# Performance work log

Hardware: AMD Instinct MI355X
Metric: run time of the kernel (lower is better)

## Reference

```python
import jax, jax.numpy as jnp
import numpy as np

IN_FEATURES = 1024
OUT_FEATURES = 256
GRID_SIZE = 5
SPLINE_ORDER = 3
SCALE_BASE = 1.0
GRID_RANGE = (-1.0, 1.0)


def make_grid():
    h = (GRID_RANGE[1] - GRID_RANGE[0]) / GRID_SIZE
    g = jnp.arange(-SPLINE_ORDER, GRID_SIZE + SPLINE_ORDER + 1, dtype=jnp.float32) * h + GRID_RANGE[0]
    # (in_features, grid_size + 2*spline_order + 1) = (1024, 12)
    return jnp.broadcast_to(g[None, :], (IN_FEATURES, g.shape[0]))


def setup_inputs() -> dict:
    key = jax.random.key(0)
    k1, k2, k3 = jax.random.split(key, 3)
    batch = 16384
    x = jax.random.normal(k1, (batch, IN_FEATURES), dtype=jnp.float32)
    base_weight = jax.random.normal(k2, (OUT_FEATURES, IN_FEATURES), dtype=jnp.float32) * 0.03
    n_basis = GRID_SIZE + SPLINE_ORDER  # 8
    spline_weight = (jax.random.uniform(k3, (OUT_FEATURES, IN_FEATURES * n_basis), dtype=jnp.float32) - 0.5) * 0.1 / n_basis
    grid = make_grid()
    return {"x": x, "base_weight": base_weight, "spline_weight": spline_weight, "grid": grid}


def b_splines(x, grid):
    # x: (B, F) -> (B, F, grid_size + spline_order)
    xe = x[:, :, None]  # (B, F, 1)
    bases = ((xe >= grid[:, :-1]) & (xe < grid[:, 1:])).astype(x.dtype)
    for k in range(1, SPLINE_ORDER + 1):
        left = (xe - grid[:, : -(k + 1)]) / (grid[:, k:-1] - grid[:, : -(k + 1)])
        right = (grid[:, k + 1 :] - xe) / (grid[:, k + 1 :] - grid[:, 1:-k])
        bases = left * bases[:, :, :-1] + right * bases[:, :, 1:]
    return bases.reshape(x.shape[0], -1)  # (B, F*(grid_size+spline_order))


def reference(x, base_weight, spline_weight, grid):
    base_out = jax.nn.silu(x) @ (base_weight * SCALE_BASE).T  # (B, out)
    spline_basis = b_splines(x, grid)                          # (B, F*8)
    spline_out = spline_basis @ spline_weight.T                # (B, out)
    return base_out + spline_out
```

## Files before the change

### kernel.cpp

```cpp
#include <hip/hip_runtime.h>
#include <cstdint>
#include <cstddef>

typedef unsigned short u16;
typedef unsigned int   u32;
typedef unsigned long long u64;
typedef __attribute__((ext_vector_type(8))) short short8;
typedef __attribute__((ext_vector_type(4))) float f32x4;

#define M_ROWS 16384
#define N_COLS 256
#define IN_F   1024
#define K_SPL  8192
#define K_TOT  9216
#define NCHUNK 144
#define SPLITK 2
#define CPB    (NCHUNK / SPLITK)

__device__ __forceinline__ u32 f2bf1(float f) {
  u32 u = __float_as_uint(f);
  u += 0x7fffu + ((u >> 16) & 1u);
  return u >> 16;
}
__device__ __forceinline__ u32 pk2(float a, float b) {
  return f2bf1(a) | (f2bf1(b) << 16);
}
__device__ __forceinline__ float silu(float v) {
  return v * __builtin_amdgcn_rcpf(1.f + __expf(-v));
}

__device__ __forceinline__ uint4 basis8(float xv) {
  float u = fmaf(xv, 2.5f, 5.5f);
  int i0 = (int)u;
  float fr = u - (float)i0;
  float fr2 = fr * fr, fr3 = fr2 * fr;
  float om  = 1.f - fr;
  float om3 = om * om * om;
  float w0 = om3 * (1.f / 6.f);
  float w3 = fr3 * (1.f / 6.f);
  float w1 = fmaf(fr3, 0.5f, fmaf(fr2, -1.f, 2.f / 3.f));
  float w2 = fmaf(fr + fr2 - fr3, 0.5f, 1.f / 6.f);
  u64 W = (u64)pk2(w0, w1) | ((u64)pk2(w2, w3) << 32);
  if (!(u >= 0.f && u < 11.f)) W = 0ull;
  int s = (i0 - 3) * 16;
  u64 lo, hi;
  if (s >= 64)      { int r = s - 64; lo = 0ull; hi = (r < 64) ? (W << r) : 0ull; }
  else if (s > 0)   { lo = W << s;    hi = W >> (64 - s); }
  else if (s == 0)  { lo = W;         hi = 0ull; }
  else              { int r = -s;     lo = (r < 64) ? (W >> r) : 0ull; hi = 0ull; }
  uint4 o;
  o.x = (u32)lo; o.y = (u32)(lo >> 32); o.z = (u32)hi; o.w = (u32)(hi >> 32);
  return o;
}

__global__ void pack_weights(const float* __restrict__ bw, const float* __restrict__ sw,
                             u16* __restrict__ Bp) {
  int o  = blockIdx.y;
  int k4 = (blockIdx.x * blockDim.x + threadIdx.x) * 4;
  const float* src = (k4 < K_SPL) ? (sw + (size_t)o * K_SPL + k4)
                                  : (bw + (size_t)o * IN_F + (k4 - K_SPL));
  float a = src[0], b = src[1], c = src[2], d = src[3];
  uint2 v; v.x = pk2(a, b); v.y = pk2(c, d);
  *(uint2*)(Bp + (size_t)o * K_TOT + k4) = v;
}

__global__ __launch_bounds__(512, 4)
void kan_gemm(const float* __restrict__ x, const u16* __restrict__ Bp,
              float* __restrict__ out) {
  __shared__ __align__(16) u16 As[64 * 64];
  __shared__ __align__(16) u16 Bs[256 * 64];

  const int tid  = threadIdx.x;
  const int lane = tid & 63;
  const int w    = tid >> 6;
  const int wm   = w & 1;
  const int wn   = w >> 1;

  const int bid  = blockIdx.x;
  const int kid  = bid & 1;
  const int mb   = bid >> 1;
  const int row0 = mb * 64;
  const int cs   = kid * CPB, c1 = cs + CPB;

  f32x4 acc[2][4];
#pragma unroll
  for (int i = 0; i < 2; ++i)
#pragma unroll
    for (int j = 0; j < 4; ++j)
      acc[i][j] = (f32x4){0.f, 0.f, 0.f, 0.f};

  const int sr = tid >> 3;
  const int sq = tid & 7;

  const int lm = lane & 15;
  const int kg = lane >> 4;
  int a_off[2][2], b_off[2][4];
#pragma unroll
  for (int h = 0; h < 2; ++h) {
    int c = h * 4 + kg;
#pragma unroll
    for (int i = 0; i < 2; ++i) {
      int ra = wm * 32 + i * 16 + lm;
      a_off[h][i] = ra * 64 + ((c ^ (ra & 7)) * 8);
    }
#pragma unroll
    for (int j = 0; j < 4; ++j) {
      int rb = wn * 64 + j * 16 + lm;
      b_off[h][j] = rb * 64 + ((c ^ (rb & 7)) * 8);
    }
  }

  float px;
  float4 pb0, pb1;

  auto LOADX = [&](int c) {
    if (c < 128) {
      px = x[(size_t)(row0 + sr) * IN_F + c * 8 + sq];
    } else {
      const float* xp = x + (size_t)(row0 + sr) * IN_F + (c - 128) * 64 + sq * 8;
      pb0 = *(const float4*)xp;
      pb1 = *(const float4*)(xp + 4);
    }
  };

  auto BUILD = [&](int c) {
    uint4 q;
    if (c < 128) {
      q = basis8(px);
    } else {
      q.x = pk2(silu(pb0.x), silu(pb0.y));
      q.y = pk2(silu(pb0.z), silu(pb0.w));
      q.z = pk2(silu(pb1.x), silu(pb1.y));
      q.w = pk2(silu(pb1.z), silu(pb1.w));
    }
    *(uint4*)(As + sr * 64 + ((sq ^ (sr & 7)) * 8)) = q;
  };

  auto STAGEB = [&](int c) {
#pragma unroll
    for (int it = 0; it < 4; ++it) {
      int s = tid + it * 512;
      int r_ = s >> 3, cc = (s & 7) ^ (r_ & 7);
      const u16* gp = Bp + (size_t)r_ * K_TOT + c * 64 + cc * 8;
      __builtin_amdgcn_global_load_lds((const __attribute__((address_space(1))) void*)gp,
                                       (__attribute__((address_space(3))) void*)(Bs + s * 8),
                                       16, 0, 0);
    }
  };

  LOADX(cs);
  for (int c = cs; c < c1; ++c) {
    BUILD(c);
    STAGEB(c);
    if (c + 1 < c1) LOADX(c + 1);
    __syncthreads();
#pragma unroll
    for (int h = 0; h < 2; ++h) {
      short8 af[2], bf[4];
#pragma unroll
      for (int i = 0; i < 2; ++i) af[i] = *(const short8*)(As + a_off[h][i]);
#pragma unroll
      for (int j = 0; j < 4; ++j) bf[j] = *(const short8*)(Bs + b_off[h][j]);
#pragma unroll
      for (int i = 0; i < 2; ++i)
#pragma unroll
        for (int j = 0; j < 4; ++j)
          acc[i][j] = __builtin_amdgcn_mfma_f32_16x16x32_bf16(af[i], bf[j], acc[i][j], 0, 0, 0);
    }
    __syncthreads();
  }

  const int lc = lane & 15;
  const int lr = (lane >> 4) * 4;
#pragma unroll
  for (int i = 0; i < 2; ++i) {
#pragma unroll
    for (int j = 0; j < 4; ++j) {
      int gr = row0 + wm * 32 + i * 16 + lr;
      int gc = wn * 64 + j * 16 + lc;
      float* po = out + (size_t)gr * N_COLS + gc;
#pragma unroll
      for (int r = 0; r < 4; ++r)
        unsafeAtomicAdd(po + (size_t)r * N_COLS, acc[i][j][r]);
    }
  }
}

extern "C" void kernel_launch(void* const* d_in, const int* in_sizes, int n_in,
                              void* d_out, int out_size, void* d_ws, size_t ws_size,
                              hipStream_t stream) {
  const float* x  = (const float*)d_in[0];
  const float* bw = (const float*)d_in[1];
  const float* sw = (const float*)d_in[2];
  float* out = (float*)d_out;
  u16* Bp = (u16*)d_ws;

  hipMemsetAsync(d_out, 0, (size_t)M_ROWS * N_COLS * sizeof(float), stream);

  dim3 pgrid(K_TOT / 4 / 256, N_COLS);
  pack_weights<<<pgrid, 256, 0, stream>>>(bw, sw, Bp);

  kan_gemm<<<512, 512, 0, stream>>>(x, Bp, out);
}
```

Baseline: 212.0 us.

## Double-buffer A and B LDS tiles to overlap staging with MFMA

Adds a second LDS buffer for the A and B tiles and restructures the K loop as a two-stage ping-pong. The next chunk's B tile (async global_load_lds) and basis/SiLU A tile are prepared while MFMAs run on the current buffer, and one of the two barriers per chunk is removed. LDS use doubles to about 80 KB per block, which may reduce how many blocks fit on a CU compared with the launch_bounds target.

```diff
diff --git a/kernel.cpp b/kernel.cpp
--- a/kernel.cpp
+++ b/kernel.cpp
@@ -67,8 +67,8 @@
 __global__ __launch_bounds__(512, 4)
 void kan_gemm(const float* __restrict__ x, const u16* __restrict__ Bp,
               float* __restrict__ out) {
-  __shared__ __align__(16) u16 As[64 * 64];
-  __shared__ __align__(16) u16 Bs[256 * 64];
+  __shared__ __align__(16) u16 Bs[2 * 256 * 64];
+  __shared__ __align__(16) u16 As[2 * 64 * 64];
 
   const int tid  = threadIdx.x;
   const int lane = tid & 63;
@@ -123,7 +123,7 @@
     }
   };
 
-  auto BUILD = [&](int c) {
+  auto BUILD = [&](int c, int buf) {
     uint4 q;
     if (c < 128) {
       q = basis8(px);
@@ -133,41 +133,58 @@
       q.z = pk2(silu(pb1.x), silu(pb1.y));
       q.w = pk2(silu(pb1.z), silu(pb1.w));
     }
-    *(uint4*)(As + sr * 64 + ((sq ^ (sr & 7)) * 8)) = q;
-  };
-
-  auto STAGEB = [&](int c) {
+    *(uint4*)(As + buf * (64 * 64) + sr * 64 + ((sq ^ (sr & 7)) * 8)) = q;
+  };
+
+  auto STAGEB = [&](int c, int buf) {
+    u16* base = Bs + buf * (256 * 64);
 #pragma unroll
     for (int it = 0; it < 4; ++it) {
       int s = tid + it * 512;
       int r_ = s >> 3, cc = (s & 7) ^ (r_ & 7);
       const u16* gp = Bp + (size_t)r_ * K_TOT + c * 64 + cc * 8;
       __builtin_amdgcn_global_load_lds((const __attribute__((address_space(1))) void*)gp,
-                                       (__attribute__((address_space(3))) void*)(Bs + s * 8),
+                                       (__attribute__((address_space(3))) void*)(base + s * 8),
                                        16, 0, 0);
     }
   };
 
-  LOADX(cs);
-  for (int c = cs; c < c1; ++c) {
-    BUILD(c);
-    STAGEB(c);
-    if (c + 1 < c1) LOADX(c + 1);
-    __syncthreads();
+  auto MFMA_PHASE = [&](int buf) {
+    const u16* Ab = As + buf * (64 * 64);
+    const u16* Bb = Bs + buf * (256 * 64);
 #pragma unroll
     for (int h = 0; h < 2; ++h) {
       short8 af[2], bf[4];
 #pragma unroll
-      for (int i = 0; i < 2; ++i) af[i] = *(const short8*)(As + a_off[h][i]);
-#pragma unroll
-      for (int j = 0; j < 4; ++j) bf[j] = *(const short8*)(Bs + b_off[h][j]);
+      for (int i = 0; i < 2; ++i) af[i] = *(const short8*)(Ab + a_off[h][i]);
+#pragma unroll
+      for (int j = 0; j < 4; ++j) bf[j] = *(const short8*)(Bb + b_off[h][j]);
 #pragma unroll
       for (int i = 0; i < 2; ++i)
 #pragma unroll
         for (int j = 0; j < 4; ++j)
           acc[i][j] = __builtin_amdgcn_mfma_f32_16x16x32_bf16(af[i], bf[j], acc[i][j], 0, 0, 0);
     }
+  };
+
+  LOADX(cs);
+  STAGEB(cs, 0);
+  BUILD(cs, 0);
+  if (cs + 1 < c1) LOADX(cs + 1);
+  __syncthreads();
+
+  for (int c = cs; c < c1; c += 2) {
+    if (c + 1 < c1) { STAGEB(c + 1, 1); BUILD(c + 1, 1); }
+    if (c + 2 < c1) LOADX(c + 2);
+    MFMA_PHASE(0);
     __syncthreads();
+
+    if (c + 1 < c1) {
+      if (c + 2 < c1) { STAGEB(c + 2, 0); BUILD(c + 2, 0); }
+      if (c + 3 < c1) LOADX(c + 3);
+      MFMA_PHASE(1);
+      __syncthreads();
+    }
   }
 
   const int lc = lane & 15;
```

Result: faster. 204.7 us (-3.5%).

## Pipeline kan_gemm with 4-stage LDS ring, 1024 threads, K=32 chunks

Applied to the files above, without the earlier changes.

Blocks grow to 1024 threads (16 waves, each computing a 32x32 tile), and the K chunk drops to 32. A 4-slot LDS ring buffer lets B staging run three chunks ahead and A basis building run two chunks ahead, split across thread quarters. This replaces the two __syncthreads per chunk with one barrier plus explicit vmcnt waits. The aim is to overlap global loads and basis computation with MFMA and to cut barrier stalls. In exchange each wave reuses less data per fragment, there are twice as many barriers overall, and the hand-written waitcnt logic adds fragility.

```diff
diff --git a/kernel.cpp b/kernel.cpp
--- a/kernel.cpp
+++ b/kernel.cpp
@@ -13,7 +13,7 @@
 #define IN_F   1024
 #define K_SPL  8192
 #define K_TOT  9216
-#define NCHUNK 144
+#define NCHUNK 288
 #define SPLITK 2
 #define CPB    (NCHUNK / SPLITK)
 
@@ -64,11 +64,11 @@
   *(uint2*)(Bp + (size_t)o * K_TOT + k4) = v;
 }
 
-__global__ __launch_bounds__(512, 4)
+__global__ __launch_bounds__(1024, 8)
 void kan_gemm(const float* __restrict__ x, const u16* __restrict__ Bp,
               float* __restrict__ out) {
-  __shared__ __align__(16) u16 As[64 * 64];
-  __shared__ __align__(16) u16 Bs[256 * 64];
+  __shared__ __align__(16) u16 Bs[4 * 256 * 32];
+  __shared__ __align__(16) u16 As[4 * 64 * 32];
 
   const int tid  = threadIdx.x;
   const int lane = tid & 63;
@@ -82,92 +82,105 @@
   const int row0 = mb * 64;
   const int cs   = kid * CPB, c1 = cs + CPB;
 
-  f32x4 acc[2][4];
+  f32x4 acc[2][2];
 #pragma unroll
   for (int i = 0; i < 2; ++i)
 #pragma unroll
-    for (int j = 0; j < 4; ++j)
+    for (int j = 0; j < 2; ++j)
       acc[i][j] = (f32x4){0.f, 0.f, 0.f, 0.f};
 
-  const int sr = tid >> 3;
-  const int sq = tid & 7;
+  const int q    = tid >> 8;
+  const int loc  = tid & 255;
+  const int brow = loc >> 2;
+  const int bq   = loc & 3;
+  const int a_wr = brow * 32 + ((bq ^ ((brow >> 1) & 3)) * 8);
 
   const int lm = lane & 15;
   const int kg = lane >> 4;
-  int a_off[2][2], b_off[2][4];
-#pragma unroll
-  for (int h = 0; h < 2; ++h) {
-    int c = h * 4 + kg;
-#pragma unroll
-    for (int i = 0; i < 2; ++i) {
-      int ra = wm * 32 + i * 16 + lm;
-      a_off[h][i] = ra * 64 + ((c ^ (ra & 7)) * 8);
-    }
-#pragma unroll
-    for (int j = 0; j < 4; ++j) {
-      int rb = wn * 64 + j * 16 + lm;
-      b_off[h][j] = rb * 64 + ((c ^ (rb & 7)) * 8);
-    }
-  }
+  int a_off[2], b_off[2];
+#pragma unroll
+  for (int i = 0; i < 2; ++i) {
+    int ra = wm * 32 + i * 16 + lm;
+    a_off[i] = ra * 32 + ((kg ^ ((ra >> 1) & 3)) * 8);
+  }
+#pragma unroll
+  for (int j = 0; j < 2; ++j) {
+    int rb = wn * 32 + j * 16 + lm;
+    b_off[j] = rb * 32 + ((kg ^ ((rb >> 1) & 3)) * 8);
+  }
+
+  const u32 stage_goff = (u32)(tid >> 2) * K_TOT + (((tid & 3) ^ ((tid >> 3) & 3)) * 8);
+  const int stage_loff = tid * 8;
 
   float px;
   float4 pb0, pb1;
 
   auto LOADX = [&](int c) {
-    if (c < 128) {
-      px = x[(size_t)(row0 + sr) * IN_F + c * 8 + sq];
+    if ((c & 3) != q) return;
+    if (c < 256) {
+      px = x[(size_t)(row0 + brow) * IN_F + c * 4 + bq];
     } else {
-      const float* xp = x + (size_t)(row0 + sr) * IN_F + (c - 128) * 64 + sq * 8;
+      const float* xp = x + (size_t)(row0 + brow) * IN_F + (c - 256) * 32 + bq * 8;
       pb0 = *(const float4*)xp;
       pb1 = *(const float4*)(xp + 4);
     }
   };
 
   auto BUILD = [&](int c) {
-    uint4 q;
-    if (c < 128) {
-      q = basis8(px);
+    if ((c & 3) != q) return;
+    uint4 v;
+    if (c < 256) {
+      v = basis8(px);
     } else {
-      q.x = pk2(silu(pb0.x), silu(pb0.y));
-      q.y = pk2(silu(pb0.z), silu(pb0.w));
-      q.z = pk2(silu(pb1.x), silu(pb1.y));
-      q.w = pk2(silu(pb1.z), silu(pb1.w));
+      v.x = pk2(silu(pb0.x), silu(pb0.y));
+      v.y = pk2(silu(pb0.z), silu(pb0.w));
+      v.z = pk2(silu(pb1.x), silu(pb1.y));
+      v.w = pk2(silu(pb1.z), silu(pb1.w));
     }
-    *(uint4*)(As + sr * 64 + ((sq ^ (sr & 7)) * 8)) = q;
+    *(uint4*)(As + (c & 3) * (64 * 32) + a_wr) = v;
   };
 
   auto STAGEB = [&](int c) {
-#pragma unroll
-    for (int it = 0; it < 4; ++it) {
-      int s = tid + it * 512;
-      int r_ = s >> 3, cc = (s & 7) ^ (r_ & 7);
-      const u16* gp = Bp + (size_t)r_ * K_TOT + c * 64 + cc * 8;
-      __builtin_amdgcn_global_load_lds((const __attribute__((address_space(1))) void*)gp,
-                                       (__attribute__((address_space(3))) void*)(Bs + s * 8),
-                                       16, 0, 0);
-    }
+    const u16* gp = Bp + stage_goff + c * 32;
+    __builtin_amdgcn_global_load_lds((const __attribute__((address_space(1))) void*)gp,
+                                     (__attribute__((address_space(3))) void*)
+                                       (Bs + (c & 3) * (256 * 32) + stage_loff),
+                                     16, 0, 0);
   };
 
-  LOADX(cs);
+  LOADX(cs); LOADX(cs + 1); LOADX(cs + 2);
+  asm volatile("s_waitcnt vmcnt(0)" ::: "memory");
+  BUILD(cs); BUILD(cs + 1); BUILD(cs + 2);
+  STAGEB(cs); STAGEB(cs + 1); STAGEB(cs + 2);
+  asm volatile("s_waitcnt vmcnt(2) lgkmcnt(0)" ::: "memory");
+  __builtin_amdgcn_s_barrier();
+
   for (int c = cs; c < c1; ++c) {
-    BUILD(c);
-    STAGEB(c);
-    if (c + 1 < c1) LOADX(c + 1);
-    __syncthreads();
-#pragma unroll
-    for (int h = 0; h < 2; ++h) {
-      short8 af[2], bf[4];
-#pragma unroll
-      for (int i = 0; i < 2; ++i) af[i] = *(const short8*)(As + a_off[h][i]);
-#pragma unroll
-      for (int j = 0; j < 4; ++j) bf[j] = *(const short8*)(Bs + b_off[h][j]);
-#pragma unroll
-      for (int i = 0; i < 2; ++i)
-#pragma unroll
-        for (int j = 0; j < 4; ++j)
-          acc[i][j] = __builtin_amdgcn_mfma_f32_16x16x32_bf16(af[i], bf[j], acc[i][j], 0, 0, 0);
-    }
-    __syncthreads();
+    const u16* Ab = As + (c & 3) * (64 * 32);
+    const u16* Bb = Bs + (c & 3) * (256 * 32);
+    short8 af[2], bf[2];
+#pragma unroll
+    for (int i = 0; i < 2; ++i) af[i] = *(const short8*)(Ab + a_off[i]);
+#pragma unroll
+    for (int j = 0; j < 2; ++j) bf[j] = *(const short8*)(Bb + b_off[j]);
+
+    if (c + 3 < c1) STAGEB(c + 3);
+    if (c + 2 < c1) BUILD(c + 2);
+    if (c + 3 < c1) LOADX(c + 3);
+
+    const int rem = c1 - c;
+    if (rem >= 4)      asm volatile("s_waitcnt vmcnt(3) lgkmcnt(0)" ::: "memory");
+    else if (rem == 3) asm volatile("s_waitcnt vmcnt(2) lgkmcnt(0)" ::: "memory");
+    else               asm volatile("s_waitcnt vmcnt(0) lgkmcnt(0)" ::: "memory");
+    __builtin_amdgcn_s_barrier();
+
+    __builtin_amdgcn_s_setprio(1);
+#pragma unroll
+    for (int i = 0; i < 2; ++i)
+#pragma unroll
+      for (int j = 0; j < 2; ++j)
+        acc[i][j] = __builtin_amdgcn_mfma_f32_16x16x32_bf16(af[i], bf[j], acc[i][j], 0, 0, 0);
+    __builtin_amdgcn_s_setprio(0);
   }
 
   const int lc = lane & 15;
@@ -175,9 +188,9 @@
 #pragma unroll
   for (int i = 0; i < 2; ++i) {
 #pragma unroll
-    for (int j = 0; j < 4; ++j) {
+    for (int j = 0; j < 2; ++j) {
       int gr = row0 + wm * 32 + i * 16 + lr;
-      int gc = wn * 64 + j * 16 + lc;
+      int gc = wn * 32 + j * 16 + lc;
       float* po = out + (size_t)gr * N_COLS + gc;
 #pragma unroll
       for (int r = 0; r < 4; ++r)
@@ -200,5 +213,5 @@
   dim3 pgrid(K_TOT / 4 / 256, N_COLS);
   pack_weights<<<pgrid, 256, 0, stream>>>(bw, sw, Bp);
 
-  kan_gemm<<<512, 512, 0, stream>>>(x, Bp, out);
-}
+  kan_gemm<<<512, 1024, 0, stream>>>(x, Bp, out);
+}
```

Result: slower. 234.2 us (+10.5%).

## Double-buffer LDS tiles and enlarge M tile to 128 rows

Applied to the files above, without the earlier changes.

The GEMM tile grows from 64 to 128 rows per block, so each block holds a 4x4 grid of MFMA accumulators per wave and the B tile is reused across twice as many rows. A and B shared-memory buffers are double-buffered: the next B tile is staged asynchronously and the next A tile is built while the current MFMAs run, using manual vmcnt waits and a single barrier per iteration. MFMA sections are raised in priority with s_setprio. The cost is more LDS and registers, which lowers occupancy, and half as many blocks (256), which may underfill the GPU's compute units.

```diff
diff --git a/kernel.cpp b/kernel.cpp
--- a/kernel.cpp
+++ b/kernel.cpp
@@ -64,11 +64,11 @@
   *(uint2*)(Bp + (size_t)o * K_TOT + k4) = v;
 }
 
-__global__ __launch_bounds__(512, 4)
+__global__ __launch_bounds__(512, 2)
 void kan_gemm(const float* __restrict__ x, const u16* __restrict__ Bp,
               float* __restrict__ out) {
-  __shared__ __align__(16) u16 As[64 * 64];
-  __shared__ __align__(16) u16 Bs[256 * 64];
+  __shared__ __align__(16) u16 Bs[2 * 256 * 64];
+  __shared__ __align__(16) u16 As[2 * 128 * 64];
 
   const int tid  = threadIdx.x;
   const int lane = tid & 63;
@@ -79,104 +79,143 @@
   const int bid  = blockIdx.x;
   const int kid  = bid & 1;
   const int mb   = bid >> 1;
-  const int row0 = mb * 64;
+  const int row0 = mb * 128;
   const int cs   = kid * CPB, c1 = cs + CPB;
 
-  f32x4 acc[2][4];
-#pragma unroll
-  for (int i = 0; i < 2; ++i)
+  f32x4 acc[4][4];
+#pragma unroll
+  for (int i = 0; i < 4; ++i)
 #pragma unroll
     for (int j = 0; j < 4; ++j)
       acc[i][j] = (f32x4){0.f, 0.f, 0.f, 0.f};
 
-  const int sr = tid >> 3;
-  const int sq = tid & 7;
+  const int br = tid >> 2;
+  const int bq = tid & 3;
+  const int a_wr0 = br * 64 + ((bq ^ (br & 7)) * 8);
+  const int a_wr1 = br * 64 + (((bq + 4) ^ (br & 7)) * 8);
 
   const int lm = lane & 15;
   const int kg = lane >> 4;
-  int a_off[2][2], b_off[2][4];
-#pragma unroll
-  for (int h = 0; h < 2; ++h) {
-    int c = h * 4 + kg;
-#pragma unroll
-    for (int i = 0; i < 2; ++i) {
-      int ra = wm * 32 + i * 16 + lm;
-      a_off[h][i] = ra * 64 + ((c ^ (ra & 7)) * 8);
-    }
-#pragma unroll
-    for (int j = 0; j < 4; ++j) {
-      int rb = wn * 64 + j * 16 + lm;
-      b_off[h][j] = rb * 64 + ((c ^ (rb & 7)) * 8);
-    }
-  }
-
-  float px;
-  float4 pb0, pb1;
+  int a_off[4], b_off[4];
+#pragma unroll
+  for (int i = 0; i < 4; ++i) {
+    int ra = wm * 64 + i * 16 + lm;
+    a_off[i] = ra * 64 + ((kg ^ (ra & 7)) * 8);
+  }
+#pragma unroll
+  for (int j = 0; j < 4; ++j) {
+    int rb = wn * 64 + j * 16 + lm;
+    b_off[j] = rb * 64 + ((kg ^ (rb & 7)) * 8);
+  }
+
+  u32 stage_goff[4];
+  int stage_loff[4];
+#pragma unroll
+  for (int it = 0; it < 4; ++it) {
+    int s  = tid + it * 512;
+    int r_ = s >> 3, cc = (s & 7) ^ (r_ & 7);
+    stage_goff[it] = (u32)r_ * K_TOT + cc * 8;
+    stage_loff[it] = s * 8;
+  }
+
+  float  px0, px1;
+  float4 pb00, pb01, pb10, pb11;
 
   auto LOADX = [&](int c) {
+    const float* xr = x + (size_t)(row0 + br) * IN_F;
     if (c < 128) {
-      px = x[(size_t)(row0 + sr) * IN_F + c * 8 + sq];
+      px0 = xr[c * 8 + bq];
+      px1 = xr[c * 8 + bq + 4];
     } else {
-      const float* xp = x + (size_t)(row0 + sr) * IN_F + (c - 128) * 64 + sq * 8;
-      pb0 = *(const float4*)xp;
-      pb1 = *(const float4*)(xp + 4);
+      const float* xp0 = xr + (c - 128) * 64 + bq * 8;
+      const float* xp1 = xr + (c - 128) * 64 + (bq + 4) * 8;
+      pb00 = *(const float4*)xp0; pb01 = *(const float4*)(xp0 + 4);
+      pb10 = *(const float4*)xp1; pb11 = *(const float4*)(xp1 + 4);
     }
   };
 
   auto BUILD = [&](int c) {
-    uint4 q;
+    u16* Ab = As + (c & 1) * (128 * 64);
+    uint4 q0, q1;
     if (c < 128) {
-      q = basis8(px);
+      q0 = basis8(px0);
+      q1 = basis8(px1);
     } else {
-      q.x = pk2(silu(pb0.x), silu(pb0.y));
-      q.y = pk2(silu(pb0.z), silu(pb0.w));
-      q.z = pk2(silu(pb1.x), silu(pb1.y));
-      q.w = pk2(silu(pb1.z), silu(pb1.w));
-    }
-    *(uint4*)(As + sr * 64 + ((sq ^ (sr & 7)) * 8)) = q;
+      q0.x = pk2(silu(pb00.x), silu(pb00.y));
+      q0.y = pk2(silu(pb00.z), silu(pb00.w));
+      q0.z = pk2(silu(pb01.x), silu(pb01.y));
+      q0.w = pk2(silu(pb01.z), silu(pb01.w));
+      q1.x = pk2(silu(pb10.x), silu(pb10.y));
+      q1.y = pk2(silu(pb10.z), silu(pb10.w));
+      q1.z = pk2(silu(pb11.x), silu(pb11.y));
+      q1.w = pk2(silu(pb11.z), silu(pb11.w));
+    }
+    *(uint4*)(Ab + a_wr0) = q0;
+    *(uint4*)(Ab + a_wr1) = q1;
   };
 
   auto STAGEB = [&](int c) {
+    u16* base = Bs + (c & 1) * (256 * 64);
 #pragma unroll
     for (int it = 0; it < 4; ++it) {
-      int s = tid + it * 512;
-      int r_ = s >> 3, cc = (s & 7) ^ (r_ & 7);
-      const u16* gp = Bp + (size_t)r_ * K_TOT + c * 64 + cc * 8;
+      const u16* gp = Bp + stage_goff[it] + c * 64;
       __builtin_amdgcn_global_load_lds((const __attribute__((address_space(1))) void*)gp,
-                                       (__attribute__((address_space(3))) void*)(Bs + s * 8),
+                                       (__attribute__((address_space(3))) void*)(base + stage_loff[it]),
                                        16, 0, 0);
     }
   };
 
   LOADX(cs);
+  STAGEB(cs);
+  BUILD(cs);
+  LOADX(cs + 1);
+  asm volatile("s_waitcnt vmcnt(2) lgkmcnt(0)" ::: "memory");
+  __builtin_amdgcn_s_barrier();
+
   for (int c = cs; c < c1; ++c) {
-    BUILD(c);
-    STAGEB(c);
-    if (c + 1 < c1) LOADX(c + 1);
-    __syncthreads();
+    if (c + 1 < c1) STAGEB(c + 1);
+
+    const u16* Ab = As + (c & 1) * (128 * 64);
+    const u16* Bb = Bs + (c & 1) * (256 * 64);
+    short8 af[2][4], bf[2][4];
 #pragma unroll
     for (int h = 0; h < 2; ++h) {
-      short8 af[2], bf[4];
-#pragma unroll
-      for (int i = 0; i < 2; ++i) af[i] = *(const short8*)(As + a_off[h][i]);
-#pragma unroll
-      for (int j = 0; j < 4; ++j) bf[j] = *(const short8*)(Bs + b_off[h][j]);
-#pragma unroll
-      for (int i = 0; i < 2; ++i)
+      const int hx = h * 32;
+#pragma unroll
+      for (int i = 0; i < 4; ++i) af[h][i] = *(const short8*)(Ab + (a_off[i] ^ hx));
+#pragma unroll
+      for (int j = 0; j < 4; ++j) bf[h][j] = *(const short8*)(Bb + (b_off[j] ^ hx));
+    }
+
+    if (c + 1 < c1) BUILD(c + 1);
+    if (c + 2 < c1) LOADX(c + 2);
+
+    __builtin_amdgcn_s_setprio(1);
+#pragma unroll
+    for (int h = 0; h < 2; ++h)
+#pragma unroll
+      for (int i = 0; i < 4; ++i)
 #pragma unroll
         for (int j = 0; j < 4; ++j)
-          acc[i][j] = __builtin_amdgcn_mfma_f32_16x16x32_bf16(af[i], bf[j], acc[i][j], 0, 0, 0);
-    }
-    __syncthreads();
+          acc[i][j] = __builtin_amdgcn_mfma_f32_16x16x32_bf16(af[h][i], bf[h][j], acc[i][j], 0, 0, 0);
+    __builtin_amdgcn_s_setprio(0);
+
+    if (c + 1 < c1) {
+      const int nx = (c + 2 < c1) ? ((c + 2 < 128) ? 2 : 4) : 0;
+      if (nx == 2)      asm volatile("s_waitcnt vmcnt(2) lgkmcnt(0)" ::: "memory");
+      else if (nx == 4) asm volatile("s_waitcnt vmcnt(4) lgkmcnt(0)" ::: "memory");
+      else              asm volatile("s_waitcnt vmcnt(0) lgkmcnt(0)" ::: "memory");
+      __builtin_amdgcn_s_barrier();
+    }
   }
 
   const int lc = lane & 15;
   const int lr = (lane >> 4) * 4;
 #pragma unroll
-  for (int i = 0; i < 2; ++i) {
+  for (int i = 0; i < 4; ++i) {
 #pragma unroll
     for (int j = 0; j < 4; ++j) {
-      int gr = row0 + wm * 32 + i * 16 + lr;
+      int gr = row0 + wm * 64 + i * 16 + lr;
       int gc = wn * 64 + j * 16 + lc;
       float* po = out + (size_t)gr * N_COLS + gc;
 #pragma unroll
@@ -200,5 +239,5 @@
   dim3 pgrid(K_TOT / 4 / 256, N_COLS);
   pack_weights<<<pgrid, 256, 0, stream>>>(bw, sw, Bp);
 
-  kan_gemm<<<512, 512, 0, stream>>>(x, Bp, out);
-}
+  kan_gemm<<<256, 512, 0, stream>>>(x, Bp, out);
+}
```

Result: slower. 241.6 us (+13.9%).
